# Performance work log

Hardware: AMD Instinct MI355X
Metric: run time of the kernel (lower is better)

The kernel has to match this reference:

```python
import jax, jax.numpy as jnp
import numpy as np

B, L_PREM, T_HYP, D = 32, 256, 128, 256


def setup_inputs() -> dict:
    key = jax.random.key(0)
    ks = jax.random.split(key, 6)
    scale = 1.0 / np.sqrt(D)
    return {
        "x": jax.random.normal(ks[0], (B, L_PREM + T_HYP, D), dtype=jnp.float32),
        "w_y": jax.random.normal(ks[1], (D, D), dtype=jnp.float32) * scale,
        "w_h": jax.random.normal(ks[2], (D, D), dtype=jnp.float32) * scale,
        "w_r": jax.random.normal(ks[3], (D, D), dtype=jnp.float32) * scale,
        "w_alpha": jax.random.normal(ks[4], (D, 1), dtype=jnp.float32) * scale,
        "w_t": jax.random.normal(ks[5], (D, D), dtype=jnp.float32) * scale,
        "L": L_PREM,
    }


def reference(x, w_y, w_h, w_r, w_alpha, w_t, L):
    # x: (B, L + T, D)
    premise = x[:, :L, :]                 # Y: (B, L, D)
    hypothesis = jnp.swapaxes(x[:, L:, :], 0, 1)  # (T, B, D)

    # Y @ W_y does not depend on t: hoist out of the scan (same math).
    WY = jnp.einsum("bld,de->ble", premise, w_y)  # (B, L, D)

    def step(r_tm1, h_t):
        # r_tm1: (B, D), h_t: (B, D)
        s = h_t @ w_h + r_tm1 @ w_r                 # (B, D)
        Mt = jnp.tanh(WY + s[:, None, :])           # (B, L, D)
        scores = jnp.squeeze(Mt @ w_alpha, -1)      # (B, L)
        alpha = jax.nn.softmax(scores, axis=-1)     # (B, L)
        r_t = jnp.einsum("bl,bld->bd", alpha, premise) + r_tm1 @ w_t
        return r_t, r_t

    r0 = jnp.zeros_like(premise[:, 0, :])           # (B, D)
    _, rs = jax.lax.scan(step, r0, hypothesis)      # rs: (T, B, D)
    return jnp.swapaxes(rs, 0, 1)                   # (B, T, D)
```

## Files before the change

### kernel.cpp

```cpp
#include <hip/hip_runtime.h>
#include <hip/hip_fp16.h>

typedef unsigned long long u64;

#define C2X 2.8853900817779268f
#define LOG2E 1.4426950408889634f

#define WYS_OFF   0u
#define PR_OFF    4194304u
#define PREMH_OFF 8388608u
#define HWH_OFF   12582912u
#define WTH_OFF   16777216u
#define WTR_OFF   16908288u
#define ZP_OFF    17039360u
#define RCH_OFF   18087936u
#define MEMSET_SZ 1179648u

#define PRC_OFF   0u
#define WTRC_OFF  16384u
#define PREMC_OFF 32768u
#define WTC_OFF   49152u
#define WYC_OFF   65536u
#define HWHC_OFF  81920u
#define SCH_OFF   98304u
#define WACH_OFF  98432u
#define AL_OFF    98560u
#define RB0_OFF   99584u
#define RB1_OFF   100608u
#define PART_OFF  101632u
#define RED_OFF   105728u
#define LDS_TOTAL 105792u

template<int MODE>
__global__ __launch_bounds__(256) void prep_gemm(const float* __restrict__ x,
                                                 const float* __restrict__ w,
                                                 float* __restrict__ outf,
                                                 __half* __restrict__ outh) {
    __shared__ float At[8][256];
    const int d = threadIdx.x;
    const int row0 = blockIdx.x * 8;
    for (int rr = 0; rr < 8; ++rr) {
        int r = row0 + rr;
        const float* src;
        if (MODE == 0 || MODE == 3) { int b = r >> 8, l = r & 255; src = x + (size_t)(b * 384 + l) * 256; }
        else if (MODE == 1)         { int t = r >> 5, bb = r & 31; src = x + (size_t)(bb * 384 + 256 + t) * 256; }
        else                        { src = x + (size_t)r * 256; }
        At[rr][d] = src[d];
    }
    __syncthreads();
    float acc[8] = {0.f,0.f,0.f,0.f,0.f,0.f,0.f,0.f};
    for (int k = 0; k < 256; k += 4) {
        float w0 = w[(size_t)(k + 0) * 256 + d];
        float w1 = w[(size_t)(k + 1) * 256 + d];
        float w2 = w[(size_t)(k + 2) * 256 + d];
        float w3 = w[(size_t)(k + 3) * 256 + d];
#pragma unroll
        for (int rr = 0; rr < 8; ++rr) {
            const float4 a = *(const float4*)&At[rr][k];
            float t0 = fmaf(a.x, w0, acc[rr]);
            t0 = fmaf(a.y, w1, t0);
            t0 = fmaf(a.z, w2, t0);
            acc[rr] = fmaf(a.w, w3, t0);
        }
    }
    for (int rr = 0; rr < 8; ++rr) {
        int r = row0 + rr;
        if (MODE == 0)      outh[(size_t)r * 256 + d] = __float2half(acc[rr] * C2X);
        else if (MODE == 1) outf[(size_t)r * 256 + d] = acc[rr] * C2X;
        else                outh[(size_t)r * 256 + d] = __float2half(acc[rr]);
    }
}

__global__ __launch_bounds__(256) void prep_cvt(const float* __restrict__ x,
                                                const float* __restrict__ wt,
                                                __half* __restrict__ prem_h,
                                                __half* __restrict__ wt_h) {
    int i = blockIdx.x * 256 + threadIdx.x;
    float4 v; __half* dst; int e;
    if (i < 524288) {
        e = i * 4; int b = e >> 16;
        v = *(const float4*)(x + (size_t)e + (size_t)b * 32768);
        dst = prem_h + e;
    } else if (i < 540672) {
        e = (i - 524288) * 4;
        v = *(const float4*)(wt + e);
        dst = wt_h + e;
    } else return;
    __half h[4] = {__float2half(v.x),__float2half(v.y),__float2half(v.z),__float2half(v.w)};
    *(uint2*)dst = *(const uint2*)h;
}

__device__ __forceinline__ u64 agent_load64(const u64* p) {
    return __hip_atomic_load(p, __ATOMIC_RELAXED, __HIP_MEMORY_SCOPE_AGENT);
}
__device__ __forceinline__ void agent_store64(u64* p, u64 v) {
    __hip_atomic_store(p, v, __ATOMIC_RELAXED, __HIP_MEMORY_SCOPE_AGENT);
}

__global__ __launch_bounds__(512, 1) void wbw_main(
    const __half* __restrict__ wys, const __half* __restrict__ prh,
    const __half* __restrict__ premh, const __half* __restrict__ wth,
    const __half* __restrict__ wtrh, const float* __restrict__ hwh,
    const float* __restrict__ walpha, float* __restrict__ out,
    u64* __restrict__ zp, u64* __restrict__ rch)
{
    extern __shared__ char lds[];
    const int tid = threadIdx.x;
    const int b = blockIdx.x >> 3, j = blockIdx.x & 7;

    float*  hwhc   = (float*)(lds + HWHC_OFF);
    float*  s_ch   = (float*)(lds + SCH_OFF);
    float*  wa_ch  = (float*)(lds + WACH_OFF);
    float*  al     = (float*)(lds + AL_OFF);
    float*  rb0    = (float*)(lds + RB0_OFF);
    float*  rb1    = (float*)(lds + RB1_OFF);
    float*  part   = (float*)(lds + PART_OFF);
    float*  red    = (float*)(lds + RED_OFF);

    {
        const int prt = tid & 3;
        for (int it = 0; it < 2; ++it) {
            int row = it * 128 + (tid >> 2);
            size_t g = (size_t)row * 256 + j * 32 + prt * 8;
            unsigned lo = (unsigned)row * 64 + (unsigned)prt * 16;
            *(uint4*)(lds + PRC_OFF   + lo) = *(const uint4*)(prh   + (size_t)b * 65536 + g);
            *(uint4*)(lds + WTRC_OFF  + lo) = *(const uint4*)(wtrh  + g);
            *(uint4*)(lds + PREMC_OFF + lo) = *(const uint4*)(premh + (size_t)b * 65536 + g);
            *(uint4*)(lds + WTC_OFF   + lo) = *(const uint4*)(wth   + g);
            *(uint4*)(lds + WYC_OFF   + lo) = *(const uint4*)(wys   + (size_t)b * 65536 + g);
        }
    }
    for (int it = 0; it < 8; ++it) {
        int idx = it * 512 + tid;
        int tt = idx >> 5, dd = idx & 31;
        hwhc[idx] = hwh[((size_t)tt * 32 + b) * 256 + j * 32 + dd];
    }
    if (tid < 32) wa_ch[tid] = walpha[j * 32 + tid] * (-2.0f * LOG2E);
    if (tid < 256) { al[tid] = 0.f; rb0[tid] = 0.f; rb1[tid] = 0.f; }
    __syncthreads();

    for (int t = 0; t <= 128; ++t) {
        {
            const int seg = tid >> 4;
            const int d0  = (tid & 15) * 2;
            const int s8  = seg & 7;
            const float* vec = (seg & 8) ? ((t & 1) ? rb0 : rb1) : al;
            const __half* mat = (const __half*)(lds + PRC_OFF + (size_t)(seg >> 3) * 16384u);
            float ax = 0.f, ay = 0.f;
#pragma unroll
            for (int i = 0; i < 32; ++i) {
                int l = s8 + i * 8;
                float v = vec[l];
                float2 mf = __half22float2(*(const __half2*)&mat[l * 32 + d0]);
                ax = fmaf(v, mf.x, ax);
                ay = fmaf(v, mf.y, ay);
            }
            part[seg * 32 + d0]     = ax;
            part[seg * 32 + d0 + 1] = ay;
        }
        __syncthreads();

        if (tid < 32) {
            if (t < 128) {
                float ss = 0.f;
#pragma unroll
                for (int k = 0; k < 16; ++k) ss += part[k * 32 + tid];
                s_ch[tid] = fmaf(ss, C2X, hwhc[t * 32 + tid]);
            }
        } else if (tid < 64) {
            const int d = tid - 32;
            float rv = 0.f;
#pragma unroll
            for (int k = 16; k < 32; ++k) rv += part[k * 32 + d];
            if (t >= 1) {
                out[((size_t)b * 128 + (t - 1)) * 256 + j * 32 + d] = rv;
                if (t < 128) {
                    u64 pk = ((u64)(unsigned)t << 32) | (u64)__float_as_uint(rv);
                    agent_store64(&rch[(size_t)((t & 1) * 32 + b) * 256 + j * 32 + d], pk);
                }
            }
        }
        __syncthreads();
        if (t == 128) break;

        {
            const int l = tid >> 1, dh = (tid & 1) << 4;
            union { uint4 u[2]; __half h[16]; } W;
            W.u[0] = *(const uint4*)(lds + WYC_OFF + (unsigned)l * 64 + (unsigned)dh * 2);
            W.u[1] = *(const uint4*)(lds + WYC_OFF + (unsigned)l * 64 + (unsigned)dh * 2 + 16);
            float acc = 0.f;
#pragma unroll
            for (int i = 0; i < 16; ++i) {
                float arg = __half2float(W.h[i]) + s_ch[dh + i];
                float u = __builtin_amdgcn_rcpf(__builtin_amdgcn_exp2f(arg) + 1.f);
                acc = fmaf(wa_ch[dh + i], u, acc);
            }
            acc += __shfl_xor(acc, 1, 64);
            if ((tid & 1) == 0) {
                u64 pk = ((u64)(unsigned)(t + 1) << 32) | (u64)__float_as_uint(acc);
                agent_store64(&zp[(size_t)(((t & 1) * 32 + b) * 8 + j) * 256 + l], pk);
            }
        }

        float ee = 0.f;
        if (tid < 256) {
            const u64* zb = zp + (size_t)((t & 1) * 32 + b) * 2048 + tid;
            u64 v0,v1,v2,v3,v4,v5,v6,v7; int tries = 0;
            for (;;) {
                v0 = agent_load64(zb);         v1 = agent_load64(zb + 256);
                v2 = agent_load64(zb + 512);   v3 = agent_load64(zb + 768);
                v4 = agent_load64(zb + 1024);  v5 = agent_load64(zb + 1280);
                v6 = agent_load64(zb + 1536);  v7 = agent_load64(zb + 1792);
                bool ok = ((unsigned)(v0 >> 32) > (unsigned)t) & ((unsigned)(v1 >> 32) > (unsigned)t)
                        & ((unsigned)(v2 >> 32) > (unsigned)t) & ((unsigned)(v3 >> 32) > (unsigned)t)
                        & ((unsigned)(v4 >> 32) > (unsigned)t) & ((unsigned)(v5 >> 32) > (unsigned)t)
                        & ((unsigned)(v6 >> 32) > (unsigned)t) & ((unsigned)(v7 >> 32) > (unsigned)t);
                if (__all(ok)) break;
                if (++tries > 2) __builtin_amdgcn_s_sleep(1);
            }
            float zs = __uint_as_float((unsigned)v0) + __uint_as_float((unsigned)v1)
                     + __uint_as_float((unsigned)v2) + __uint_as_float((unsigned)v3)
                     + __uint_as_float((unsigned)v4) + __uint_as_float((unsigned)v5)
                     + __uint_as_float((unsigned)v6) + __uint_as_float((unsigned)v7);
            ee = __builtin_amdgcn_exp2f(zs);
            float sv = ee;
#pragma unroll
            for (int off = 32; off; off >>= 1) sv += __shfl_xor(sv, off, 64);
            if ((tid & 63) == 0) red[tid >> 6] = sv;

            const u64* rp = &rch[(size_t)((t & 1) * 32 + b) * 256 + tid];
            u64 rv;
            for (;;) {
                rv = agent_load64(rp);
                if (__all((unsigned)(rv >> 32) >= (unsigned)t)) break;
                __builtin_amdgcn_s_sleep(1);
            }
            float* rbN = (t & 1) ? rb1 : rb0;
            rbN[tid] = __uint_as_float((unsigned)rv);
        }
        __syncthreads();
        if (tid < 256) {
            float denom = red[0] + red[1] + red[2] + red[3];
            al[tid] = ee * __builtin_amdgcn_rcpf(denom);
        }
        __syncthreads();
    }
}

extern "C" void kernel_launch(void* const* d_in, const int* in_sizes, int n_in,
                              void* d_out, int out_size, void* d_ws, size_t ws_size,
                              hipStream_t stream) {
    const float* x   = (const float*)d_in[0];
    const float* wy  = (const float*)d_in[1];
    const float* wh  = (const float*)d_in[2];
    const float* wr  = (const float*)d_in[3];
    const float* wal = (const float*)d_in[4];
    const float* wt  = (const float*)d_in[5];

    char* ws = (char*)d_ws;
    __half* wys    = (__half*)(ws + WYS_OFF);
    __half* prh    = (__half*)(ws + PR_OFF);
    __half* premh  = (__half*)(ws + PREMH_OFF);
    float*  hwh    = (float*)(ws + HWH_OFF);
    __half* wth    = (__half*)(ws + WTH_OFF);
    __half* wtrh   = (__half*)(ws + WTR_OFF);
    u64*    zp     = (u64*)(ws + ZP_OFF);
    u64*    rch    = (u64*)(ws + RCH_OFF);

    hipFuncSetAttribute((const void*)wbw_main,
                        hipFuncAttributeMaxDynamicSharedMemorySize, (int)LDS_TOTAL);

    prep_gemm<0><<<1024, 256, 0, stream>>>(x,  wy, nullptr, wys);
    prep_gemm<1><<<512,  256, 0, stream>>>(x,  wh, hwh, nullptr);
    prep_gemm<3><<<1024, 256, 0, stream>>>(x,  wr, nullptr, prh);
    prep_gemm<2><<<32,   256, 0, stream>>>(wt, wr, nullptr, wtrh);
    prep_cvt<<<2112, 256, 0, stream>>>(x, wt, premh, wth);
    hipMemsetAsync(ws + ZP_OFF, 0, MEMSET_SZ, stream);

    wbw_main<<<256, 512, LDS_TOTAL, stream>>>(wys, prh, premh, wth, wtrh, hwh,
                                              wal, (float*)d_out, zp, rch);
}
```

Measured before the change: 550.1 us.

## Fuse prep kernels and defer softmax normalisation into the recurrence step

Merges the five preprocessing launches into a single kernel. The mode-0 blocks now compute the premise products with W_y and W_r together, so the premise tile is loaded once. In the main recurrent kernel the softmax weights are kept unnormalised and the denominator is applied later via double-buffered partial sums, which drops one block barrier per step. The two matvec phases are also reorganised so the projection for step t and the r_t readout each use all 512 threads with a padded partial buffer. This shortens the serial per-step critical path at the cost of more intricate parity-indexed state.

```diff
diff --git a/kernel.cpp b/kernel.cpp
--- a/kernel.cpp
+++ b/kernel.cpp
@@ -25,69 +25,92 @@
 #define SCH_OFF   98304u
 #define WACH_OFF  98432u
 #define AL_OFF    98560u
-#define RB0_OFF   99584u
-#define RB1_OFF   100608u
-#define PART_OFF  101632u
-#define RED_OFF   105728u
-#define LDS_TOTAL 105792u
-
-template<int MODE>
-__global__ __launch_bounds__(256) void prep_gemm(const float* __restrict__ x,
-                                                 const float* __restrict__ w,
-                                                 float* __restrict__ outf,
-                                                 __half* __restrict__ outh) {
+#define RB_OFF    99584u
+#define PART_OFF  100608u
+#define RED_OFF   104832u
+#define LDS_TOTAL 104864u
+
+__global__ __launch_bounds__(256) void prep_all(const float* __restrict__ x,
+                                                const float* __restrict__ wy,
+                                                const float* __restrict__ wh,
+                                                const float* __restrict__ wr,
+                                                const float* __restrict__ wt,
+                                                __half* __restrict__ wys,
+                                                __half* __restrict__ prh,
+                                                float* __restrict__ hwh,
+                                                __half* __restrict__ wtrh,
+                                                __half* __restrict__ premh,
+                                                __half* __restrict__ wth) {
+    const int blk = blockIdx.x;
+    if (blk >= 1568) {
+        int i = (blk - 1568) * 256 + threadIdx.x;
+        float4 v; __half* dst; int e;
+        if (i < 524288) {
+            e = i * 4; int b = e >> 16;
+            v = *(const float4*)(x + (size_t)e + (size_t)b * 32768);
+            dst = premh + e;
+        } else if (i < 540672) {
+            e = (i - 524288) * 4;
+            v = *(const float4*)(wt + e);
+            dst = wth + e;
+        } else return;
+        __half h[4] = {__float2half(v.x),__float2half(v.y),__float2half(v.z),__float2half(v.w)};
+        *(uint2*)dst = *(const uint2*)h;
+        return;
+    }
     __shared__ float At[8][256];
     const int d = threadIdx.x;
-    const int row0 = blockIdx.x * 8;
+    int mode, row0;
+    if (blk < 1024)      { mode = 0; row0 = blk * 8; }
+    else if (blk < 1536) { mode = 1; row0 = (blk - 1024) * 8; }
+    else                 { mode = 2; row0 = (blk - 1536) * 8; }
     for (int rr = 0; rr < 8; ++rr) {
         int r = row0 + rr;
         const float* src;
-        if (MODE == 0 || MODE == 3) { int b = r >> 8, l = r & 255; src = x + (size_t)(b * 384 + l) * 256; }
-        else if (MODE == 1)         { int t = r >> 5, bb = r & 31; src = x + (size_t)(bb * 384 + 256 + t) * 256; }
-        else                        { src = x + (size_t)r * 256; }
+        if (mode == 0)      { int b = r >> 8, l = r & 255; src = x + (size_t)(b * 384 + l) * 256; }
+        else if (mode == 1) { int tt = r >> 5, bb = r & 31; src = x + (size_t)(bb * 384 + 256 + tt) * 256; }
+        else                { src = wt + (size_t)r * 256; }
         At[rr][d] = src[d];
     }
     __syncthreads();
-    float acc[8] = {0.f,0.f,0.f,0.f,0.f,0.f,0.f,0.f};
-    for (int k = 0; k < 256; k += 4) {
-        float w0 = w[(size_t)(k + 0) * 256 + d];
-        float w1 = w[(size_t)(k + 1) * 256 + d];
-        float w2 = w[(size_t)(k + 2) * 256 + d];
-        float w3 = w[(size_t)(k + 3) * 256 + d];
-#pragma unroll
+    if (mode == 0) {
+        float accy[8] = {0,0,0,0,0,0,0,0}, accr[8] = {0,0,0,0,0,0,0,0};
+        for (int k = 0; k < 256; k += 2) {
+            float y0 = wy[(size_t)k * 256 + d], y1 = wy[(size_t)(k + 1) * 256 + d];
+            float r0 = wr[(size_t)k * 256 + d], r1 = wr[(size_t)(k + 1) * 256 + d];
+#pragma unroll
+            for (int rr = 0; rr < 8; ++rr) {
+                float2 a = *(const float2*)&At[rr][k];
+                accy[rr] = fmaf(a.x, y0, accy[rr]); accy[rr] = fmaf(a.y, y1, accy[rr]);
+                accr[rr] = fmaf(a.x, r0, accr[rr]); accr[rr] = fmaf(a.y, r1, accr[rr]);
+            }
+        }
         for (int rr = 0; rr < 8; ++rr) {
-            const float4 a = *(const float4*)&At[rr][k];
-            float t0 = fmaf(a.x, w0, acc[rr]);
-            t0 = fmaf(a.y, w1, t0);
-            t0 = fmaf(a.z, w2, t0);
-            acc[rr] = fmaf(a.w, w3, t0);
-        }
-    }
-    for (int rr = 0; rr < 8; ++rr) {
-        int r = row0 + rr;
-        if (MODE == 0)      outh[(size_t)r * 256 + d] = __float2half(acc[rr] * C2X);
-        else if (MODE == 1) outf[(size_t)r * 256 + d] = acc[rr] * C2X;
-        else                outh[(size_t)r * 256 + d] = __float2half(acc[rr]);
-    }
-}
-
-__global__ __launch_bounds__(256) void prep_cvt(const float* __restrict__ x,
-                                                const float* __restrict__ wt,
-                                                __half* __restrict__ prem_h,
-                                                __half* __restrict__ wt_h) {
-    int i = blockIdx.x * 256 + threadIdx.x;
-    float4 v; __half* dst; int e;
-    if (i < 524288) {
-        e = i * 4; int b = e >> 16;
-        v = *(const float4*)(x + (size_t)e + (size_t)b * 32768);
-        dst = prem_h + e;
-    } else if (i < 540672) {
-        e = (i - 524288) * 4;
-        v = *(const float4*)(wt + e);
-        dst = wt_h + e;
-    } else return;
-    __half h[4] = {__float2half(v.x),__float2half(v.y),__float2half(v.z),__float2half(v.w)};
-    *(uint2*)dst = *(const uint2*)h;
+            int r = row0 + rr;
+            wys[(size_t)r * 256 + d] = __float2half(accy[rr] * C2X);
+            prh[(size_t)r * 256 + d] = __float2half(accr[rr]);
+        }
+    } else {
+        const float* w = (mode == 1) ? wh : wr;
+        float acc[8] = {0,0,0,0,0,0,0,0};
+        for (int k = 0; k < 256; k += 4) {
+            float w0 = w[(size_t)k * 256 + d], w1 = w[(size_t)(k+1) * 256 + d];
+            float w2 = w[(size_t)(k+2) * 256 + d], w3 = w[(size_t)(k+3) * 256 + d];
+#pragma unroll
+            for (int rr = 0; rr < 8; ++rr) {
+                float4 a = *(const float4*)&At[rr][k];
+                float t0 = fmaf(a.x, w0, acc[rr]);
+                t0 = fmaf(a.y, w1, t0);
+                t0 = fmaf(a.z, w2, t0);
+                acc[rr] = fmaf(a.w, w3, t0);
+            }
+        }
+        for (int rr = 0; rr < 8; ++rr) {
+            int r = row0 + rr;
+            if (mode == 1) hwh[(size_t)r * 256 + d] = acc[rr] * C2X;
+            else           wtrh[(size_t)r * 256 + d] = __float2half(acc[rr]);
+        }
+    }
 }
 
 __device__ __forceinline__ u64 agent_load64(const u64* p) {
@@ -108,14 +131,13 @@
     const int tid = threadIdx.x;
     const int b = blockIdx.x >> 3, j = blockIdx.x & 7;
 
-    float*  hwhc   = (float*)(lds + HWHC_OFF);
-    float*  s_ch   = (float*)(lds + SCH_OFF);
-    float*  wa_ch  = (float*)(lds + WACH_OFF);
-    float*  al     = (float*)(lds + AL_OFF);
-    float*  rb0    = (float*)(lds + RB0_OFF);
-    float*  rb1    = (float*)(lds + RB1_OFF);
-    float*  part   = (float*)(lds + PART_OFF);
-    float*  red    = (float*)(lds + RED_OFF);
+    float* hwhc  = (float*)(lds + HWHC_OFF);
+    float* s_ch  = (float*)(lds + SCH_OFF);
+    float* wa_ch = (float*)(lds + WACH_OFF);
+    float* al    = (float*)(lds + AL_OFF);
+    float* rb    = (float*)(lds + RB_OFF);
+    float* part  = (float*)(lds + PART_OFF);
+    float* red   = (float*)(lds + RED_OFF);
 
     {
         const int prt = tid & 3;
@@ -136,75 +158,98 @@
         hwhc[idx] = hwh[((size_t)tt * 32 + b) * 256 + j * 32 + dd];
     }
     if (tid < 32) wa_ch[tid] = walpha[j * 32 + tid] * (-2.0f * LOG2E);
-    if (tid < 256) { al[tid] = 0.f; rb0[tid] = 0.f; rb1[tid] = 0.f; }
+    if (tid < 256) { al[tid] = 0.f; rb[tid] = 0.f; }
+    if (tid < 8)   red[tid] = (tid == 0 || tid == 4) ? 1.f : 0.f;
     __syncthreads();
 
     for (int t = 0; t <= 128; ++t) {
+        const int par = t & 1;
+        if (t < 128) {
+            {
+                const int half_ = tid >> 8;
+                const int s16 = (tid >> 4) & 15;
+                const int d0 = (tid & 15) * 2;
+                const __half* mat = (const __half*)(lds + (half_ ? WTRC_OFF : PRC_OFF));
+                const float* vec = half_ ? rb : al;
+                float ax = 0.f, ay = 0.f;
+#pragma unroll
+                for (int i = 0; i < 16; ++i) {
+                    int l = s16 + i * 16;
+                    float v = vec[l];
+                    float2 mf = __half22float2(*(const __half2*)&mat[l * 32 + d0]);
+                    ax = fmaf(v, mf.x, ax); ay = fmaf(v, mf.y, ay);
+                }
+                const int row = half_ * 16 + s16;
+                part[row * 33 + d0] = ax; part[row * 33 + d0 + 1] = ay;
+            }
+            __syncthreads();
+            if (tid < 32) {
+                const float* rd = red + (par ^ 1) * 4;
+                float rD = __builtin_amdgcn_rcpf(rd[0] + rd[1] + rd[2] + rd[3]);
+                float se = 0.f, sr = 0.f;
+#pragma unroll
+                for (int s2 = 0; s2 < 16; ++s2) {
+                    se += part[s2 * 33 + tid];
+                    sr += part[(16 + s2) * 33 + tid];
+                }
+                s_ch[tid] = fmaf(fmaf(se, rD, sr), C2X, hwhc[t * 32 + tid]);
+            }
+            __syncthreads();
+            {
+                const int l = tid >> 1, dh = (tid & 1) << 4;
+                union { uint4 u[2]; __half h[16]; } W;
+                W.u[0] = *(const uint4*)(lds + WYC_OFF + (unsigned)l * 64 + (unsigned)dh * 2);
+                W.u[1] = *(const uint4*)(lds + WYC_OFF + (unsigned)l * 64 + (unsigned)dh * 2 + 16);
+                float acc = 0.f;
+#pragma unroll
+                for (int i = 0; i < 16; ++i) {
+                    float arg = __half2float(W.h[i]) + s_ch[dh + i];
+                    float u = __builtin_amdgcn_rcpf(__builtin_amdgcn_exp2f(arg) + 1.f);
+                    acc = fmaf(wa_ch[dh + i], u, acc);
+                }
+                acc += __shfl_xor(acc, 1, 64);
+                if ((tid & 1) == 0) {
+                    u64 pk = ((u64)(unsigned)(t + 1) << 32) | (u64)__float_as_uint(acc);
+                    agent_store64(&zp[(size_t)((par * 32 + b) * 8 + j) * 256 + l], pk);
+                }
+            }
+        }
         {
-            const int seg = tid >> 4;
-            const int d0  = (tid & 15) * 2;
-            const int s8  = seg & 7;
-            const float* vec = (seg & 8) ? ((t & 1) ? rb0 : rb1) : al;
-            const __half* mat = (const __half*)(lds + PRC_OFF + (size_t)(seg >> 3) * 16384u);
+            const int half_ = tid >> 8;
+            const int s16 = (tid >> 4) & 15;
+            const int d0 = (tid & 15) * 2;
+            const __half* mat = (const __half*)(lds + (half_ ? WTC_OFF : PREMC_OFF));
+            const float* vec = half_ ? rb : al;
             float ax = 0.f, ay = 0.f;
 #pragma unroll
-            for (int i = 0; i < 32; ++i) {
-                int l = s8 + i * 8;
+            for (int i = 0; i < 16; ++i) {
+                int l = s16 + i * 16;
                 float v = vec[l];
                 float2 mf = __half22float2(*(const __half2*)&mat[l * 32 + d0]);
-                ax = fmaf(v, mf.x, ax);
-                ay = fmaf(v, mf.y, ay);
-            }
-            part[seg * 32 + d0]     = ax;
-            part[seg * 32 + d0 + 1] = ay;
+                ax = fmaf(v, mf.x, ax); ay = fmaf(v, mf.y, ay);
+            }
+            const int row = half_ * 16 + s16;
+            part[row * 33 + d0] = ax; part[row * 33 + d0 + 1] = ay;
         }
         __syncthreads();
-
-        if (tid < 32) {
+        if (tid >= 448 && tid < 480) {
+            const int d = tid - 448;
+            const float* rd = red + (par ^ 1) * 4;
+            float rD = __builtin_amdgcn_rcpf(rd[0] + rd[1] + rd[2] + rd[3]);
+            float se = 0.f, sr = 0.f;
+#pragma unroll
+            for (int s2 = 0; s2 < 16; ++s2) {
+                se += part[s2 * 33 + d];
+                sr += part[(16 + s2) * 33 + d];
+            }
+            float rv = fmaf(se, rD, sr);
+            if (t >= 1) out[((size_t)b * 128 + (t - 1)) * 256 + j * 32 + d] = rv;
             if (t < 128) {
-                float ss = 0.f;
-#pragma unroll
-                for (int k = 0; k < 16; ++k) ss += part[k * 32 + tid];
-                s_ch[tid] = fmaf(ss, C2X, hwhc[t * 32 + tid]);
-            }
-        } else if (tid < 64) {
-            const int d = tid - 32;
-            float rv = 0.f;
-#pragma unroll
-            for (int k = 16; k < 32; ++k) rv += part[k * 32 + d];
-            if (t >= 1) {
-                out[((size_t)b * 128 + (t - 1)) * 256 + j * 32 + d] = rv;
-                if (t < 128) {
-                    u64 pk = ((u64)(unsigned)t << 32) | (u64)__float_as_uint(rv);
-                    agent_store64(&rch[(size_t)((t & 1) * 32 + b) * 256 + j * 32 + d], pk);
-                }
-            }
-        }
-        __syncthreads();
-        if (t == 128) break;
-
-        {
-            const int l = tid >> 1, dh = (tid & 1) << 4;
-            union { uint4 u[2]; __half h[16]; } W;
-            W.u[0] = *(const uint4*)(lds + WYC_OFF + (unsigned)l * 64 + (unsigned)dh * 2);
-            W.u[1] = *(const uint4*)(lds + WYC_OFF + (unsigned)l * 64 + (unsigned)dh * 2 + 16);
-            float acc = 0.f;
-#pragma unroll
-            for (int i = 0; i < 16; ++i) {
-                float arg = __half2float(W.h[i]) + s_ch[dh + i];
-                float u = __builtin_amdgcn_rcpf(__builtin_amdgcn_exp2f(arg) + 1.f);
-                acc = fmaf(wa_ch[dh + i], u, acc);
-            }
-            acc += __shfl_xor(acc, 1, 64);
-            if ((tid & 1) == 0) {
-                u64 pk = ((u64)(unsigned)(t + 1) << 32) | (u64)__float_as_uint(acc);
-                agent_store64(&zp[(size_t)(((t & 1) * 32 + b) * 8 + j) * 256 + l], pk);
-            }
-        }
-
-        float ee = 0.f;
-        if (tid < 256) {
-            const u64* zb = zp + (size_t)((t & 1) * 32 + b) * 2048 + tid;
+                u64 pk = ((u64)(unsigned)t << 32) | (u64)__float_as_uint(rv);
+                agent_store64(&rch[(size_t)(par * 32 + b) * 256 + j * 32 + d], pk);
+            }
+        } else if (tid < 256 && t < 128) {
+            const u64* zb = zp + (size_t)(par * 32 + b) * 2048 + tid;
             u64 v0,v1,v2,v3,v4,v5,v6,v7; int tries = 0;
             for (;;) {
                 v0 = agent_load64(zb);         v1 = agent_load64(zb + 256);
@@ -222,26 +267,20 @@
                      + __uint_as_float((unsigned)v2) + __uint_as_float((unsigned)v3)
                      + __uint_as_float((unsigned)v4) + __uint_as_float((unsigned)v5)
                      + __uint_as_float((unsigned)v6) + __uint_as_float((unsigned)v7);
-            ee = __builtin_amdgcn_exp2f(zs);
+            float ee = __builtin_amdgcn_exp2f(zs);
             float sv = ee;
 #pragma unroll
             for (int off = 32; off; off >>= 1) sv += __shfl_xor(sv, off, 64);
-            if ((tid & 63) == 0) red[tid >> 6] = sv;
-
-            const u64* rp = &rch[(size_t)((t & 1) * 32 + b) * 256 + tid];
+            if ((tid & 63) == 0) red[par * 4 + (tid >> 6)] = sv;
+            const u64* rp = &rch[(size_t)(par * 32 + b) * 256 + tid];
             u64 rv;
             for (;;) {
                 rv = agent_load64(rp);
                 if (__all((unsigned)(rv >> 32) >= (unsigned)t)) break;
                 __builtin_amdgcn_s_sleep(1);
             }
-            float* rbN = (t & 1) ? rb1 : rb0;
-            rbN[tid] = __uint_as_float((unsigned)rv);
-        }
-        __syncthreads();
-        if (tid < 256) {
-            float denom = red[0] + red[1] + red[2] + red[3];
-            al[tid] = ee * __builtin_amdgcn_rcpf(denom);
+            rb[tid] = __uint_as_float((unsigned)rv);
+            al[tid] = ee;
         }
         __syncthreads();
     }
@@ -270,11 +309,7 @@
     hipFuncSetAttribute((const void*)wbw_main,
                         hipFuncAttributeMaxDynamicSharedMemorySize, (int)LDS_TOTAL);
 
-    prep_gemm<0><<<1024, 256, 0, stream>>>(x,  wy, nullptr, wys);
-    prep_gemm<1><<<512,  256, 0, stream>>>(x,  wh, hwh, nullptr);
-    prep_gemm<3><<<1024, 256, 0, stream>>>(x,  wr, nullptr, prh);
-    prep_gemm<2><<<32,   256, 0, stream>>>(wt, wr, nullptr, wtrh);
-    prep_cvt<<<2112, 256, 0, stream>>>(x, wt, premh, wth);
+    prep_all<<<3680, 256, 0, stream>>>(x, wy, wh, wr, wt, wys, prh, hwh, wtrh, premh, wth);
     hipMemsetAsync(ws + ZP_OFF, 0, MEMSET_SZ, stream);
 
     wbw_main<<<256, 512, LDS_TOTAL, stream>>>(wys, prh, premh, wth, wtrh, hwh,
```

New measurement: 448.8 us. 18.4% less time.
